# Kernel optimization log

Measured on AMD Instinct MI355X. Metric: run time of the kernel, lower is better.

The kernel has to match this reference:

```python
import jax, jax.numpy as jnp
import numpy as np

E, H, I, R, T, TOPK = 8, 1024, 2816, 8, 4096, 2
SCALING = 2.0  # lora_alpha / r = 16 / 8


def setup_inputs() -> dict:
    key = jax.random.key(0)
    ks = jax.random.split(key, 12)
    inp = {
        "hidden_states": jax.random.normal(ks[0], (T, H), dtype=jnp.float32),
        "routing_weights": jax.random.uniform(ks[1], (T, TOPK), dtype=jnp.float32),
        "selected_experts": jax.random.randint(ks[2], (T, TOPK), 0, E),
        # frozen base expert weights, (G, K, N) layout
        "gate_proj": jax.random.normal(ks[3], (E, H, I), dtype=jnp.float32) * 0.02,
        "up_proj": jax.random.normal(ks[4], (E, H, I), dtype=jnp.float32) * 0.02,
        "down_proj": jax.random.normal(ks[5], (E, I, H), dtype=jnp.float32) * 0.02,
        # LoRA adapters, A: [E, in, r], B: [E, r, out]  (B random, not zero, so delta is exercised)
        "gate_A": jax.random.normal(ks[6], (E, H, R), dtype=jnp.float32) * 0.02,
        "gate_B": jax.random.normal(ks[7], (E, R, I), dtype=jnp.float32) * 0.02,
        "up_A": jax.random.normal(ks[8], (E, H, R), dtype=jnp.float32) * 0.02,
        "up_B": jax.random.normal(ks[9], (E, R, I), dtype=jnp.float32) * 0.02,
        "down_A": jax.random.normal(ks[10], (E, I, R), dtype=jnp.float32) * 0.02,
        "down_B": jax.random.normal(ks[11], (E, R, H), dtype=jnp.float32) * 0.02,
    }
    return inp


def _moe_lora_forward(x, routing_weights, selected_experts,
                      gate_proj, up_proj, down_proj,
                      gate_A, gate_B, up_A, up_B, down_A, down_B):
    # combine weights per (token, expert): [T, E]
    combine = jnp.sum(
        jax.nn.one_hot(selected_experts, E, dtype=x.dtype) * routing_weights[..., None],
        axis=1,
    )
    out = jnp.zeros_like(x)
    for e in range(E):  # static small loop over experts
        g = x @ gate_proj[e] + SCALING * ((x @ gate_A[e]) @ gate_B[e])
        u = x @ up_proj[e] + SCALING * ((x @ up_A[e]) @ up_B[e])
        h = jax.nn.silu(g) * u  # [T, I]
        y = h @ down_proj[e] + SCALING * ((h @ down_A[e]) @ down_B[e])  # [T, H]
        out = out + combine[:, e:e + 1] * y
    return out


def reference(hidden_states, routing_weights, selected_experts,
              gate_proj, up_proj, down_proj,
              gate_A, gate_B, up_A, up_B, down_A, down_B):
    return _moe_lora_forward(hidden_states, routing_weights, selected_experts,
                             gate_proj, up_proj, down_proj,
                             gate_A, gate_B, up_A, up_B, down_A, down_B)
```

## Files before the change

kernel.cpp:

```cpp
#include <hip/hip_runtime.h>
#include <stdint.h>

#define T_TOK 4096
#define NE 8
#define HH 1024
#define II 2816
#define HE 1056
#define IEW 2944
#define HT 23
#define RRK 8
#define NPAIR (T_TOK*2)
#define ROWCAP 10240
#define MT_MAX 40
#define SCAL 2.0f

typedef short v8s __attribute__((ext_vector_type(8)));
typedef float v4f __attribute__((ext_vector_type(4)));

__device__ __forceinline__ unsigned short f2bf(float f){
  union { float f; unsigned u; } c; c.f = f;
  unsigned u = c.u;
  u += 0x7FFFu + ((u >> 16) & 1u);
  return (unsigned short)(u >> 16);
}
__device__ __forceinline__ float bf2f(unsigned short h){
  union { unsigned u; float f; } c; c.u = ((unsigned)h) << 16;
  return c.f;
}
__device__ __forceinline__ void gload16(const void* g, void* l){
  __builtin_amdgcn_global_load_lds(
      (const __attribute__((address_space(1))) unsigned int*)g,
      (__attribute__((address_space(3))) unsigned int*)l, 16, 0, 0);
}
__device__ __forceinline__ void fence_(){ asm volatile("" ::: "memory"); }

__global__ void route_count(const int* __restrict__ sel, int* __restrict__ counts,
                            int* __restrict__ bases, int* __restrict__ tile_e,
                            int* __restrict__ tile_r0){
  __shared__ int c[NE];
  int tid = threadIdx.x;
  if (tid < NE) c[tid] = 0;
  __syncthreads();
  for (int p = tid; p < NPAIR; p += 256) atomicAdd(&c[sel[p]], 1);
  __syncthreads();
  if (tid == 0){
    int b = 0;
    for (int e = 0; e < NE; e++){ counts[e] = c[e]; bases[e] = b; b += ((c[e] + 255) >> 8) << 8; }
    bases[NE] = b;
    int t = 0;
    for (int e = 0; e < NE; e++){
      int nt = (c[e] + 255) >> 8;
      for (int i = 0; i < nt; i++){ tile_e[t] = e; tile_r0[t] = bases[e] + i * 256; t++; }
    }
    for (; t < MT_MAX; t++){ tile_e[t] = -1; tile_r0[t] = 0; }
  }
}

__global__ void route_fill(const int* __restrict__ sel, const float* __restrict__ rw,
                           const int* __restrict__ bases,
                           int* __restrict__ row_token, int* __restrict__ row_expert,
                           float* __restrict__ row_w, int* __restrict__ pair2row){
  int e = blockIdx.x;
  int lane = threadIdx.x;
  if (e == NE){
    for (int idx = bases[NE] + lane; idx < ROWCAP; idx += 64){
      row_token[idx] = -1; row_expert[idx] = 0; row_w[idx] = 0.f;
    }
    return;
  }
  int base = bases[e];
  int cnt = 0;
  for (int chunk = 0; chunk < NPAIR; chunk += 64){
    int p = chunk + lane;
    bool m = (sel[p] == e);
    unsigned long long mask = __ballot(m);
    if (m){
      int pos = __popcll(mask & ((1ull << lane) - 1ull));
      int dst = base + cnt + pos;
      row_token[dst] = p >> 1;
      row_expert[dst] = e;
      row_w[dst] = rw[p];
      pair2row[p] = dst;
    }
    cnt += __popcll(mask);
  }
  int nb = bases[e + 1];
  for (int idx = base + cnt + lane; idx < nb; idx += 64){
    row_token[idx] = -1; row_expert[idx] = e; row_w[idx] = 0.f;
  }
}

__device__ __forceinline__ void transpose_body(const float* __restrict__ W,
                                               unsigned short* __restrict__ Wt,
                                               int K, int N, int KE, int e, int bid){
  int tilesK = K >> 6;
  int kt = (bid % tilesK) * 64;
  int nt = (bid / tilesK) * 64;
  __shared__ float tile[64][65];
  int tid = threadIdx.x;
  int r = tid >> 2;
  int c0 = (tid & 3) * 16;
  const float* src = W + (size_t)e * K * N + (size_t)(kt + r) * N + nt + c0;
  #pragma unroll
  for (int i = 0; i < 4; i++){
    float4 v = *(const float4*)(src + i * 4);
    tile[r][c0 + i*4 + 0] = v.x; tile[r][c0 + i*4 + 1] = v.y;
    tile[r][c0 + i*4 + 2] = v.z; tile[r][c0 + i*4 + 3] = v.w;
  }
  __syncthreads();
  union { unsigned short us[16]; uint4 q[2]; } pk;
  #pragma unroll
  for (int j = 0; j < 16; j++) pk.us[j] = f2bf(tile[c0 + j][r]);
  unsigned short* dst = Wt + (size_t)e * N * KE + (size_t)(nt + r) * KE + kt + c0;
  *(uint4*)(dst) = pk.q[0];
  *(uint4*)(dst + 8) = pk.q[1];
}

__global__ void wprep(const float* __restrict__ gate_proj, const float* __restrict__ up_proj,
                      const float* __restrict__ down_proj,
                      const float* __restrict__ gB, const float* __restrict__ uB,
                      const float* __restrict__ dB,
                      unsigned short* __restrict__ Wtg, unsigned short* __restrict__ Wtu,
                      unsigned short* __restrict__ Wtd){
  int b = blockIdx.x;
  if (b < 5632){
    transpose_body(gate_proj, Wtg, HH, II, HE, b / 704, b % 704);
  } else if (b < 11264){
    b -= 5632;
    transpose_body(up_proj, Wtu, HH, II, HE, b / 704, b % 704);
  } else if (b < 16896){
    b -= 11264;
    transpose_body(down_proj, Wtd, II, HH, IEW, b / 704, b % 704);
  } else if (b < 16984){
    int idx = (b - 16896) * 256 + threadIdx.x;
    if (idx >= NE * II) return;
    int e = idx / II, n = idx % II;
    unsigned short* g = Wtg + ((size_t)e * II + n) * HE + HH;
    unsigned short* u = Wtu + ((size_t)e * II + n) * HE + HH;
    #pragma unroll
    for (int j = 0; j < 8; j++){
      g[j] = f2bf(gB[((size_t)e * RRK + j) * II + n]);
      u[j] = 0;
      g[8 + j] = 0;
      u[8 + j] = f2bf(uB[((size_t)e * RRK + j) * II + n]);
    }
    #pragma unroll
    for (int j = 16; j < 32; j++){ g[j] = 0; u[j] = 0; }
  } else {
    int idx = (b - 16984) * 256 + threadIdx.x;
    if (idx >= NE * HH) return;
    int e = idx / HH, n = idx % HH;
    unsigned short* d = Wtd + ((size_t)e * HH + n) * IEW + II;
    #pragma unroll
    for (int j = 0; j < 8; j++) d[j] = f2bf(dB[((size_t)e * RRK + j) * HH + n]);
    for (int j = 8; j < 128; j++) d[j] = 0;
  }
}

__global__ void gxa_kernel(const float* __restrict__ x, const float* __restrict__ gA,
                           const float* __restrict__ uA, const int* __restrict__ row_token,
                           const int* __restrict__ row_expert,
                           unsigned short* __restrict__ Xg){
  int p = blockIdx.x; int tid = threadIdx.x;
  int tok = row_token[p]; int e = row_expert[p];
  int k0 = tid * 4;
  float4 xv = make_float4(0.f, 0.f, 0.f, 0.f);
  if (tok >= 0) xv = *(const float4*)(x + (size_t)tok * HH + k0);
  uint2 o;
  o.x = (unsigned)f2bf(xv.x) | ((unsigned)f2bf(xv.y) << 16);
  o.y = (unsigned)f2bf(xv.z) | ((unsigned)f2bf(xv.w) << 16);
  *(uint2*)(Xg + (size_t)p * HE + k0) = o;

  float ag[8], au[8];
  #pragma unroll
  for (int r = 0; r < 8; r++){ ag[r] = 0.f; au[r] = 0.f; }
  if (tok >= 0){
    const float* pg = gA + ((size_t)e * HH + k0) * RRK;
    const float* pu = uA + ((size_t)e * HH + k0) * RRK;
    float xs[4] = {xv.x, xv.y, xv.z, xv.w};
    #pragma unroll
    for (int j = 0; j < 4; j++){
      #pragma unroll
      for (int r = 0; r < 8; r++){
        ag[r] += xs[j] * pg[j * RRK + r];
        au[r] += xs[j] * pu[j * RRK + r];
      }
    }
  }
  __shared__ float redg[8][4], redu[8][4];
  int lane = tid & 63, wv = tid >> 6;
  #pragma unroll
  for (int r = 0; r < 8; r++){
    float v1 = ag[r], v2 = au[r];
    for (int off = 32; off > 0; off >>= 1){ v1 += __shfl_down(v1, off); v2 += __shfl_down(v2, off); }
    if (lane == 0){ redg[r][wv] = v1; redu[r][wv] = v2; }
  }
  __syncthreads();
  if (tid < 8)
    Xg[(size_t)p * HE + HH + tid] = f2bf(SCAL * (redg[tid][0] + redg[tid][1] + redg[tid][2] + redg[tid][3]));
  else if (tid < 16){
    int r = tid - 8;
    Xg[(size_t)p * HE + HH + 8 + r] = f2bf(SCAL * (redu[r][0] + redu[r][1] + redu[r][2] + redu[r][3]));
  } else if (tid < 32){
    Xg[(size_t)p * HE + HH + tid] = 0;
  }
}

__global__ void ha_kernel(const unsigned short* __restrict__ hbuf, const float* __restrict__ dA,
                          const int* __restrict__ row_expert, unsigned short* __restrict__ hout){
  int p = blockIdx.x; int tid = threadIdx.x;
  int e = row_expert[p];
  float a[8];
  #pragma unroll
  for (int r = 0; r < 8; r++) a[r] = 0.f;
  for (int i = 0; i < 11; i++){
    int k = i * 256 + tid;
    float hv = bf2f(hbuf[(size_t)(k >> 7) * (ROWCAP * 128) + (size_t)p * 128 + (k & 127)]);
    const float* pd = dA + ((size_t)e * II + k) * RRK;
    #pragma unroll
    for (int r = 0; r < 8; r++) a[r] += hv * pd[r];
  }
  __shared__ float red[8][4];
  int lane = tid & 63, wv = tid >> 6;
  #pragma unroll
  for (int r = 0; r < 8; r++){
    float v = a[r];
    for (int off = 32; off > 0; off >>= 1) v += __shfl_down(v, off);
    if (lane == 0) red[r][wv] = v;
  }
  __syncthreads();
  unsigned short* ext = hout + (size_t)22 * (ROWCAP * 128) + (size_t)p * 128;
  if (tid < 8)
    ext[tid] = f2bf(SCAL * (red[tid][0] + red[tid][1] + red[tid][2] + red[tid][3]));
  else if (tid < 128)
    ext[tid] = 0;
}

__launch_bounds__(512, 2)
__global__ void gemm1_kernel(const unsigned short* __restrict__ Xg,
                             const unsigned short* __restrict__ Wtg,
                             const unsigned short* __restrict__ Wtu,
                             const int* __restrict__ tile_e,
                             const int* __restrict__ tile_r0,
                             unsigned short* __restrict__ hbuf){
  int hw = blockIdx.x;
  int lg = (hw & 7) * 110 + (hw >> 3);
  int mt = lg / 22;
  int n0 = (lg % 22) * 128;

  int e = tile_e[mt];
  if (e < 0) return;
  int row0 = tile_r0[mt];

  __shared__ unsigned short lds[2][4 * 4096];
  int tid = threadIdx.x;
  int lane = tid & 63;
  int w = tid >> 6;
  int wm = w >> 1;
  int wn = w & 1;
  int g = lane >> 4, r16 = lane & 15;

  const unsigned short* srcA = Xg + (size_t)row0 * HE;
  const unsigned short* srcG = Wtg + ((size_t)e * II + n0) * HE;
  const unsigned short* srcU = Wtu + ((size_t)e * II + n0) * HE;

  v4f accg[4][4], accu[4][4];
  #pragma unroll
  for (int i = 0; i < 4; i++)
    #pragma unroll
    for (int j = 0; j < 4; j++){
      accg[i][j] = (v4f){0.f, 0.f, 0.f, 0.f};
      accu[i][j] = (v4f){0.f, 0.f, 0.f, 0.f};
    }

  int uA0 = tid, uA1 = tid + 512;
  int rA0 = uA0 >> 2, rA1 = uA1 >> 2;
  size_t gA0 = (size_t)rA0 * HE + ((uA0 & 3) ^ ((rA0 >> 1) & 3)) * 8;
  size_t gA1 = (size_t)rA1 * HE + ((uA1 & 3) ^ ((rA1 >> 1) & 3)) * 8;
  int lA0 = (uA0 & ~63) * 8, lA1 = (uA1 & ~63) * 8;
  int rB = tid >> 2;
  size_t gB = (size_t)rB * HE + ((tid & 3) ^ ((rB >> 1) & 3)) * 8;
  int lB = (tid & ~63) * 8;

  const int NT = HE / 32;

  {
    unsigned short* buf = lds[0];
    gload16(srcA + gA0, buf + lA0);
    gload16(srcA + gA1, buf + lA1);
    gload16(srcG + gB, buf + 8192 + lB);
    gload16(srcU + gB, buf + 12288 + lB);
  }

  for (int t = 0; t < NT; t++){
    if (t + 1 < NT){
      unsigned short* nbuf = lds[(t + 1) & 1];
      int ks = (t + 1) * 32;
      gload16(srcA + gA0 + ks, nbuf + lA0);
      gload16(srcA + gA1 + ks, nbuf + lA1);
      gload16(srcG + gB + ks, nbuf + 8192 + lB);
      gload16(srcU + gB + ks, nbuf + 12288 + lB);
      asm volatile("s_waitcnt vmcnt(4)" ::: "memory");
    } else {
      asm volatile("s_waitcnt vmcnt(0)" ::: "memory");
    }
    __builtin_amdgcn_s_barrier();
    fence_();
    const unsigned short* buf = lds[t & 1];
    v8s a[4], bg[4], bu[4];
    #pragma unroll
    for (int f = 0; f < 4; f++){
      int rowA = wm * 64 + f * 16 + r16;
      int ca = g ^ ((rowA >> 1) & 3);
      a[f] = *(const v8s*)(buf + rowA * 32 + ca * 8);
      int rowB = wn * 64 + f * 16 + r16;
      int cb = g ^ ((rowB >> 1) & 3);
      bg[f] = *(const v8s*)(buf + 8192 + rowB * 32 + cb * 8);
      bu[f] = *(const v8s*)(buf + 12288 + rowB * 32 + cb * 8);
    }
    #pragma unroll
    for (int fm = 0; fm < 4; fm++)
      #pragma unroll
      for (int fn = 0; fn < 4; fn++){
        accg[fm][fn] = __builtin_amdgcn_mfma_f32_16x16x32_bf16(a[fm], bg[fn], accg[fm][fn], 0, 0, 0);
        accu[fm][fn] = __builtin_amdgcn_mfma_f32_16x16x32_bf16(a[fm], bu[fn], accu[fm][fn], 0, 0, 0);
      }
    fence_();
    __builtin_amdgcn_s_barrier();
    fence_();
  }

  unsigned short* sh = (unsigned short*)lds;
  #pragma unroll
  for (int fm = 0; fm < 4; fm++)
    #pragma unroll
    for (int fn = 0; fn < 4; fn++)
      #pragma unroll
      for (int r = 0; r < 4; r++){
        int lrow = wm * 64 + fm * 16 + g * 4 + r;
        int lcol = wn * 64 + fn * 16 + r16;
        float gg = accg[fm][fn][r];
        float uu = accu[fm][fn][r];
        float hh = (gg / (1.f + __expf(-gg))) * uu;
        int ch = (lcol >> 3) ^ (lrow & 7);
        sh[lrow * 128 + ch * 8 + (lcol & 7)] = f2bf(hh);
      }
  __syncthreads();
  unsigned short* dst = hbuf + ((size_t)(n0 >> 7) * ROWCAP + row0) * 128;
  #pragma unroll
  for (int pass = 0; pass < 8; pass++){
    int idx2 = pass * 512 + tid;
    int row = idx2 >> 4;
    int ch = idx2 & 15;
    int chs = ch ^ (row & 7);
    v8s val = *(const v8s*)(sh + row * 128 + chs * 8);
    *(v8s*)(dst + row * 128 + ch * 8) = val;
  }
}

__launch_bounds__(512, 2)
__global__ void gemm2_kernel(const unsigned short* __restrict__ hbuf,
                             const unsigned short* __restrict__ Wtd,
                             const int* __restrict__ tile_e,
                             const int* __restrict__ tile_r0,
                             const float* __restrict__ row_w,
                             float* __restrict__ Y){
  int hw = blockIdx.x;
  int lg = (hw & 7) * 20 + (hw >> 3);
  int mt = lg / 4;
  int n0 = (lg % 4) * 256;

  int e = tile_e[mt];
  if (e < 0) return;
  int row0 = tile_r0[mt];

  __shared__ unsigned short lds[2][2 * 8192];
  int tid = threadIdx.x;
  int lane = tid & 63;
  int w = tid >> 6;
  int wm = w >> 1;
  int wn = w & 1;
  int g = lane >> 4, r16 = lane & 15;

  const unsigned short* srcA = hbuf + (size_t)row0 * 128;
  const unsigned short* srcB = Wtd + ((size_t)e * HH + n0) * IEW;

  v4f acc[4][8];
  #pragma unroll
  for (int i = 0; i < 4; i++)
    #pragma unroll
    for (int j = 0; j < 8; j++) acc[i][j] = (v4f){0.f, 0.f, 0.f, 0.f};

  int u0 = tid, u1 = tid + 512;
  int r0_ = u0 >> 2, r1_ = u1 >> 2;
  int c0_ = (u0 & 3) ^ ((r0_ >> 1) & 3), c1_ = (u1 & 3) ^ ((r1_ >> 1) & 3);
  size_t aoff0 = (size_t)r0_ * 128 + c0_ * 8;
  size_t aoff1 = (size_t)r1_ * 128 + c1_ * 8;
  size_t boff0 = (size_t)r0_ * IEW + c0_ * 8;
  size_t boff1 = (size_t)r1_ * IEW + c1_ * 8;
  int l0 = (u0 & ~63) * 8, l1 = (u1 & ~63) * 8;

  const int NT = IEW / 32;

  auto stage = [&](int t, unsigned short* buf){
    int ks = t * 32;
    size_t abase = (size_t)(ks >> 7) * (ROWCAP * 128) + (ks & 127);
    gload16(srcA + abase + aoff0, buf + l0);
    gload16(srcA + abase + aoff1, buf + l1);
    gload16(srcB + (size_t)ks + boff0, buf + 8192 + l0);
    gload16(srcB + (size_t)ks + boff1, buf + 8192 + l1);
  };

  stage(0, lds[0]);

  for (int t = 0; t < NT; t++){
    if (t + 1 < NT){
      stage(t + 1, lds[(t + 1) & 1]);
      asm volatile("s_waitcnt vmcnt(4)" ::: "memory");
    } else {
      asm volatile("s_waitcnt vmcnt(0)" ::: "memory");
    }
    __builtin_amdgcn_s_barrier();
    fence_();
    const unsigned short* buf = lds[t & 1];
    v8s a[4], b[8];
    #pragma unroll
    for (int f = 0; f < 4; f++){
      int rowA = wm * 64 + f * 16 + r16;
      int ca = g ^ ((rowA >> 1) & 3);
      a[f] = *(const v8s*)(buf + rowA * 32 + ca * 8);
    }
    #pragma unroll
    for (int fn = 0; fn < 8; fn++){
      int rowB = wn * 128 + fn * 16 + r16;
      int cb = g ^ ((rowB >> 1) & 3);
      b[fn] = *(const v8s*)(buf + 8192 + rowB * 32 + cb * 8);
    }
    #pragma unroll
    for (int fm = 0; fm < 4; fm++)
      #pragma unroll
      for (int fn = 0; fn < 8; fn++)
        acc[fm][fn] = __builtin_amdgcn_mfma_f32_16x16x32_bf16(a[fm], b[fn], acc[fm][fn], 0, 0, 0);
    fence_();
    __builtin_amdgcn_s_barrier();
    fence_();
  }

  #pragma unroll
  for (int fm = 0; fm < 4; fm++){
    #pragma unroll
    for (int r = 0; r < 4; r++){
      int lrow = wm * 64 + fm * 16 + g * 4 + r;
      int grow = row0 + lrow;
      float wgt = row_w[grow];
      #pragma unroll
      for (int fn = 0; fn < 8; fn++){
        int lcol = wn * 128 + fn * 16 + r16;
        Y[(size_t)grow * HH + n0 + lcol] = wgt * acc[fm][fn][r];
      }
    }
  }
}

__global__ void combine_kernel(const float* __restrict__ Y, const int* __restrict__ pair2row,
                               float* __restrict__ out){
  int t = blockIdx.x;
  int c = threadIdx.x * 4;
  int r0 = pair2row[2 * t];
  int r1 = pair2row[2 * t + 1];
  float4 a = *(const float4*)(Y + (size_t)r0 * HH + c);
  float4 b = *(const float4*)(Y + (size_t)r1 * HH + c);
  float4 o = make_float4(a.x + b.x, a.y + b.y, a.z + b.z, a.w + b.w);
  *(float4*)(out + (size_t)t * HH + c) = o;
}

extern "C" void kernel_launch(void* const* d_in, const int* in_sizes, int n_in,
                              void* d_out, int out_size, void* d_ws, size_t ws_size,
                              hipStream_t stream){
  const float* x         = (const float*)d_in[0];
  const float* rw        = (const float*)d_in[1];
  const int*   sel       = (const int*)d_in[2];
  const float* gate_proj = (const float*)d_in[3];
  const float* up_proj   = (const float*)d_in[4];
  const float* down_proj = (const float*)d_in[5];
  const float* gate_A    = (const float*)d_in[6];
  const float* gate_B    = (const float*)d_in[7];
  const float* up_A      = (const float*)d_in[8];
  const float* up_B      = (const float*)d_in[9];
  const float* down_A    = (const float*)d_in[10];
  const float* down_B    = (const float*)d_in[11];
  float* out = (float*)d_out;
  char* ws = (char*)d_ws;

  constexpr size_t OFF_COUNTS = 0;
  constexpr size_t OFF_BASES  = 256;
  constexpr size_t OFF_TILE_E = 512;
  constexpr size_t OFF_TILE_R0 = 1024;
  constexpr size_t OFF_ROWTOK = 2048;
  constexpr size_t OFF_ROWEXP = OFF_ROWTOK + (size_t)ROWCAP * 4;
  constexpr size_t OFF_ROWW   = OFF_ROWEXP + (size_t)ROWCAP * 4;
  constexpr size_t OFF_P2R    = OFF_ROWW + (size_t)ROWCAP * 4;
  constexpr size_t OFF_XG     = OFF_P2R + (size_t)NPAIR * 4;
  constexpr size_t OFF_H      = OFF_XG + (size_t)ROWCAP * HE * 2;
  constexpr size_t OFF_WTG    = OFF_H + (size_t)HT * ROWCAP * 128 * 2;
  constexpr size_t OFF_WTU    = OFF_WTG + (size_t)NE * II * HE * 2;
  constexpr size_t OFF_WTD    = OFF_WTU + (size_t)NE * II * HE * 2;
  constexpr size_t OFF_Y      = OFF_WTG;

  int* counts    = (int*)(ws + OFF_COUNTS);
  int* bases     = (int*)(ws + OFF_BASES);
  int* tile_e    = (int*)(ws + OFF_TILE_E);
  int* tile_r0   = (int*)(ws + OFF_TILE_R0);
  int* row_token = (int*)(ws + OFF_ROWTOK);
  int* row_expert= (int*)(ws + OFF_ROWEXP);
  float* row_w   = (float*)(ws + OFF_ROWW);
  int* pair2row  = (int*)(ws + OFF_P2R);
  unsigned short* Xg   = (unsigned short*)(ws + OFF_XG);
  unsigned short* hbuf = (unsigned short*)(ws + OFF_H);
  unsigned short* Wtg  = (unsigned short*)(ws + OFF_WTG);
  unsigned short* Wtu  = (unsigned short*)(ws + OFF_WTU);
  unsigned short* Wtd  = (unsigned short*)(ws + OFF_WTD);
  float* Y = (float*)(ws + OFF_Y);

  route_count<<<1, 256, 0, stream>>>(sel, counts, bases, tile_e, tile_r0);
  route_fill<<<NE + 1, 64, 0, stream>>>(sel, rw, bases, row_token, row_expert, row_w, pair2row);
  wprep<<<17016, 256, 0, stream>>>(gate_proj, up_proj, down_proj, gate_B, up_B, down_B,
                                   Wtg, Wtu, Wtd);
  gxa_kernel<<<ROWCAP, 256, 0, stream>>>(x, gate_A, up_A, row_token, row_expert, Xg);
  gemm1_kernel<<<MT_MAX * (II / 128), 512, 0, stream>>>(Xg, Wtg, Wtu, tile_e, tile_r0, hbuf);
  ha_kernel<<<ROWCAP, 256, 0, stream>>>(hbuf, down_A, row_expert, hbuf);
  gemm2_kernel<<<MT_MAX * (HH / 256), 512, 0, stream>>>(hbuf, Wtd, tile_e, tile_r0, row_w, Y);
  combine_kernel<<<T_TOK, 256, 0, stream>>>(Y, pair2row, out);
}
```

Before: 539.5 us.

## Split-K the down-projection GEMM into bf16 partials and merge gxa into wprep

The down-projection GEMM is split four ways along K, which quadruples the number of blocks so that only 160 tiles no longer underfill the GPU. Each split writes bf16 partial results, and the combine kernel sums the four partials for both expert rows. The gxa work is also folded into the wprep launch as extra blocks, removing one kernel launch and letting the two run concurrently. The cost is extra partial-output traffic and precision loss from rounding the partials to bf16. It also adds a workspace aliasing risk, since Y4 now needs four bf16 slices in the region at OFF_WTG.

```diff
diff --git a/kernel.cpp b/kernel.cpp
--- a/kernel.cpp
+++ b/kernel.cpp
@@ -121,7 +121,10 @@
                       const float* __restrict__ gB, const float* __restrict__ uB,
                       const float* __restrict__ dB,
                       unsigned short* __restrict__ Wtg, unsigned short* __restrict__ Wtu,
-                      unsigned short* __restrict__ Wtd){
+                      unsigned short* __restrict__ Wtd,
+                      const float* __restrict__ x, const float* __restrict__ gA,
+                      const float* __restrict__ uA, const int* __restrict__ row_token,
+                      const int* __restrict__ row_expert, unsigned short* __restrict__ Xg){
   int b = blockIdx.x;
   if (b < 5632){
     transpose_body(gate_proj, Wtg, HH, II, HE, b / 704, b % 704);
@@ -146,7 +149,7 @@
     }
     #pragma unroll
     for (int j = 16; j < 32; j++){ g[j] = 0; u[j] = 0; }
-  } else {
+  } else if (b < 17016){
     int idx = (b - 16984) * 256 + threadIdx.x;
     if (idx >= NE * HH) return;
     int e = idx / HH, n = idx % HH;
@@ -154,55 +157,51 @@
     #pragma unroll
     for (int j = 0; j < 8; j++) d[j] = f2bf(dB[((size_t)e * RRK + j) * HH + n]);
     for (int j = 8; j < 128; j++) d[j] = 0;
-  }
-}
-
-__global__ void gxa_kernel(const float* __restrict__ x, const float* __restrict__ gA,
-                           const float* __restrict__ uA, const int* __restrict__ row_token,
-                           const int* __restrict__ row_expert,
-                           unsigned short* __restrict__ Xg){
-  int p = blockIdx.x; int tid = threadIdx.x;
-  int tok = row_token[p]; int e = row_expert[p];
-  int k0 = tid * 4;
-  float4 xv = make_float4(0.f, 0.f, 0.f, 0.f);
-  if (tok >= 0) xv = *(const float4*)(x + (size_t)tok * HH + k0);
-  uint2 o;
-  o.x = (unsigned)f2bf(xv.x) | ((unsigned)f2bf(xv.y) << 16);
-  o.y = (unsigned)f2bf(xv.z) | ((unsigned)f2bf(xv.w) << 16);
-  *(uint2*)(Xg + (size_t)p * HE + k0) = o;
-
-  float ag[8], au[8];
-  #pragma unroll
-  for (int r = 0; r < 8; r++){ ag[r] = 0.f; au[r] = 0.f; }
-  if (tok >= 0){
-    const float* pg = gA + ((size_t)e * HH + k0) * RRK;
-    const float* pu = uA + ((size_t)e * HH + k0) * RRK;
-    float xs[4] = {xv.x, xv.y, xv.z, xv.w};
-    #pragma unroll
-    for (int j = 0; j < 4; j++){
+  } else {
+    int p = b - 17016;
+    int tid = threadIdx.x;
+    int tok = row_token[p]; int e = row_expert[p];
+    int k0 = tid * 4;
+    float4 xv = make_float4(0.f, 0.f, 0.f, 0.f);
+    if (tok >= 0) xv = *(const float4*)(x + (size_t)tok * HH + k0);
+    uint2 o;
+    o.x = (unsigned)f2bf(xv.x) | ((unsigned)f2bf(xv.y) << 16);
+    o.y = (unsigned)f2bf(xv.z) | ((unsigned)f2bf(xv.w) << 16);
+    *(uint2*)(Xg + (size_t)p * HE + k0) = o;
+
+    float ag[8], au[8];
+    #pragma unroll
+    for (int r = 0; r < 8; r++){ ag[r] = 0.f; au[r] = 0.f; }
+    if (tok >= 0){
+      const float* pg = gA + ((size_t)e * HH + k0) * RRK;
+      const float* pu = uA + ((size_t)e * HH + k0) * RRK;
+      float xs[4] = {xv.x, xv.y, xv.z, xv.w};
       #pragma unroll
-      for (int r = 0; r < 8; r++){
-        ag[r] += xs[j] * pg[j * RRK + r];
-        au[r] += xs[j] * pu[j * RRK + r];
+      for (int j = 0; j < 4; j++){
+        #pragma unroll
+        for (int r = 0; r < 8; r++){
+          ag[r] += xs[j] * pg[j * RRK + r];
+          au[r] += xs[j] * pu[j * RRK + r];
+        }
       }
     }
-  }
-  __shared__ float redg[8][4], redu[8][4];
-  int lane = tid & 63, wv = tid >> 6;
-  #pragma unroll
-  for (int r = 0; r < 8; r++){
-    float v1 = ag[r], v2 = au[r];
-    for (int off = 32; off > 0; off >>= 1){ v1 += __shfl_down(v1, off); v2 += __shfl_down(v2, off); }
-    if (lane == 0){ redg[r][wv] = v1; redu[r][wv] = v2; }
-  }
-  __syncthreads();
-  if (tid < 8)
-    Xg[(size_t)p * HE + HH + tid] = f2bf(SCAL * (redg[tid][0] + redg[tid][1] + redg[tid][2] + redg[tid][3]));
-  else if (tid < 16){
-    int r = tid - 8;
-    Xg[(size_t)p * HE + HH + 8 + r] = f2bf(SCAL * (redu[r][0] + redu[r][1] + redu[r][2] + redu[r][3]));
-  } else if (tid < 32){
-    Xg[(size_t)p * HE + HH + tid] = 0;
+    __shared__ float redg[8][4], redu[8][4];
+    int lane = tid & 63, wv = tid >> 6;
+    #pragma unroll
+    for (int r = 0; r < 8; r++){
+      float v1 = ag[r], v2 = au[r];
+      for (int off = 32; off > 0; off >>= 1){ v1 += __shfl_down(v1, off); v2 += __shfl_down(v2, off); }
+      if (lane == 0){ redg[r][wv] = v1; redu[r][wv] = v2; }
+    }
+    __syncthreads();
+    if (tid < 8)
+      Xg[(size_t)p * HE + HH + tid] = f2bf(SCAL * (redg[tid][0] + redg[tid][1] + redg[tid][2] + redg[tid][3]));
+    else if (tid < 16){
+      int r = tid - 8;
+      Xg[(size_t)p * HE + HH + 8 + r] = f2bf(SCAL * (redu[r][0] + redu[r][1] + redu[r][2] + redu[r][3]));
+    } else if (tid < 32){
+      Xg[(size_t)p * HE + HH + tid] = 0;
+    }
   }
 }
 
@@ -364,11 +363,13 @@
                              const int* __restrict__ tile_e,
                              const int* __restrict__ tile_r0,
                              const float* __restrict__ row_w,
-                             float* __restrict__ Y){
+                             unsigned short* __restrict__ Y4){
   int hw = blockIdx.x;
-  int lg = (hw & 7) * 20 + (hw >> 3);
-  int mt = lg / 4;
-  int n0 = (lg % 4) * 256;
+  int lg = (hw & 7) * 80 + (hw >> 3);
+  int mt = lg / 16;
+  int rem = lg % 16;
+  int n0 = (rem >> 2) * 256;
+  int q = rem & 3;
 
   int e = tile_e[mt];
   if (e < 0) return;
@@ -400,7 +401,9 @@
   size_t boff1 = (size_t)r1_ * IEW + c1_ * 8;
   int l0 = (u0 & ~63) * 8, l1 = (u1 & ~63) * 8;
 
-  const int NT = IEW / 32;
+  const int NQ = (IEW / 32) / 4;
+  int tbeg = q * NQ;
+  int tend = tbeg + NQ;
 
   auto stage = [&](int t, unsigned short* buf){
     int ks = t * 32;
@@ -411,10 +414,10 @@
     gload16(srcB + (size_t)ks + boff1, buf + 8192 + l1);
   };
 
-  stage(0, lds[0]);
-
-  for (int t = 0; t < NT; t++){
-    if (t + 1 < NT){
+  stage(tbeg, lds[tbeg & 1]);
+
+  for (int t = tbeg; t < tend; t++){
+    if (t + 1 < tend){
       stage(t + 1, lds[(t + 1) & 1]);
       asm volatile("s_waitcnt vmcnt(4)" ::: "memory");
     } else {
@@ -446,6 +449,7 @@
     fence_();
   }
 
+  unsigned short* Yh = Y4 + (size_t)q * ROWCAP * HH;
   #pragma unroll
   for (int fm = 0; fm < 4; fm++){
     #pragma unroll
@@ -456,22 +460,31 @@
       #pragma unroll
       for (int fn = 0; fn < 8; fn++){
         int lcol = wn * 128 + fn * 16 + r16;
-        Y[(size_t)grow * HH + n0 + lcol] = wgt * acc[fm][fn][r];
+        Yh[(size_t)grow * HH + n0 + lcol] = f2bf(wgt * acc[fm][fn][r]);
       }
     }
   }
 }
 
-__global__ void combine_kernel(const float* __restrict__ Y, const int* __restrict__ pair2row,
+__global__ void combine_kernel(const unsigned short* __restrict__ Y4,
+                               const int* __restrict__ pair2row,
                                float* __restrict__ out){
   int t = blockIdx.x;
   int c = threadIdx.x * 4;
   int r0 = pair2row[2 * t];
   int r1 = pair2row[2 * t + 1];
-  float4 a = *(const float4*)(Y + (size_t)r0 * HH + c);
-  float4 b = *(const float4*)(Y + (size_t)r1 * HH + c);
-  float4 o = make_float4(a.x + b.x, a.y + b.y, a.z + b.z, a.w + b.w);
-  *(float4*)(out + (size_t)t * HH + c) = o;
+  float s0 = 0.f, s1 = 0.f, s2 = 0.f, s3 = 0.f;
+  #pragma unroll
+  for (int q = 0; q < 4; q++){
+    const unsigned short* Yh = Y4 + (size_t)q * ROWCAP * HH;
+    uint2 a = *(const uint2*)(Yh + (size_t)r0 * HH + c);
+    uint2 b = *(const uint2*)(Yh + (size_t)r1 * HH + c);
+    s0 += bf2f((unsigned short)(a.x & 0xffff)) + bf2f((unsigned short)(b.x & 0xffff));
+    s1 += bf2f((unsigned short)(a.x >> 16))    + bf2f((unsigned short)(b.x >> 16));
+    s2 += bf2f((unsigned short)(a.y & 0xffff)) + bf2f((unsigned short)(b.y & 0xffff));
+    s3 += bf2f((unsigned short)(a.y >> 16))    + bf2f((unsigned short)(b.y >> 16));
+  }
+  *(float4*)(out + (size_t)t * HH + c) = make_float4(s0, s1, s2, s3);
 }
 
 extern "C" void kernel_launch(void* const* d_in, const int* in_sizes, int n_in,
@@ -520,15 +533,15 @@
   unsigned short* Wtg  = (unsigned short*)(ws + OFF_WTG);
   unsigned short* Wtu  = (unsigned short*)(ws + OFF_WTU);
   unsigned short* Wtd  = (unsigned short*)(ws + OFF_WTD);
-  float* Y = (float*)(ws + OFF_Y);
+  unsigned short* Y4 = (unsigned short*)(ws + OFF_Y);
 
   route_count<<<1, 256, 0, stream>>>(sel, counts, bases, tile_e, tile_r0);
   route_fill<<<NE + 1, 64, 0, stream>>>(sel, rw, bases, row_token, row_expert, row_w, pair2row);
-  wprep<<<17016, 256, 0, stream>>>(gate_proj, up_proj, down_proj, gate_B, up_B, down_B,
-                                   Wtg, Wtu, Wtd);
-  gxa_kernel<<<ROWCAP, 256, 0, stream>>>(x, gate_A, up_A, row_token, row_expert, Xg);
+  wprep<<<17016 + ROWCAP, 256, 0, stream>>>(gate_proj, up_proj, down_proj, gate_B, up_B, down_B,
+                                            Wtg, Wtu, Wtd, x, gate_A, up_A,
+                                            row_token, row_expert, Xg);
   gemm1_kernel<<<MT_MAX * (II / 128), 512, 0, stream>>>(Xg, Wtg, Wtu, tile_e, tile_r0, hbuf);
   ha_kernel<<<ROWCAP, 256, 0, stream>>>(hbuf, down_A, row_expert, hbuf);
-  gemm2_kernel<<<MT_MAX * (HH / 256), 512, 0, stream>>>(hbuf, Wtd, tile_e, tile_r0, row_w, Y);
-  combine_kernel<<<T_TOK, 256, 0, stream>>>(Y, pair2row, out);
-}
+  gemm2_kernel<<<MT_MAX * (HH / 256) * 4, 512, 0, stream>>>(hbuf, Wtd, tile_e, tile_r0, row_w, Y4);
+  combine_kernel<<<T_TOK, 256, 0, stream>>>(Y4, pair2row, out);
+}
```

Result: faster. 518.6 us (-3.9%).
